# Kernel tuning notes

Hardware: AMD Instinct MI355X
Metric: run time of the kernel (lower is better)

## Reference

```python
import jax, jax.numpy as jnp
import numpy as np

NUM_USERS = 100000
NUM_ITEMS = 50000
N_NODES = NUM_USERS + NUM_ITEMS
EMBED_K = 64
N_LAYERS = 3
N_EDGES = 2000000
BATCH = 4096
EPS = 1e-12
NEG_SLOPE = 0.01  # torch.nn.functional.leaky_relu default


def setup_inputs() -> dict:
    key = jax.random.key(0)
    ks = jax.random.split(key, 12)
    return {
        "Gu": jax.random.normal(ks[0], (NUM_USERS, EMBED_K), jnp.float32) * 0.1,
        "Gi": jax.random.normal(ks[1], (NUM_ITEMS, EMBED_K), jnp.float32) * 0.1,
        "W1": jax.random.normal(ks[2], (N_LAYERS, EMBED_K, EMBED_K), jnp.float32) * 0.1,
        "b1": jax.random.normal(ks[3], (N_LAYERS, EMBED_K), jnp.float32) * 0.1,
        "W2": jax.random.normal(ks[4], (N_LAYERS, EMBED_K, EMBED_K), jnp.float32) * 0.1,
        "b2": jax.random.normal(ks[5], (N_LAYERS, EMBED_K), jnp.float32) * 0.1,
        "edge_w": jax.random.uniform(ks[6], (N_EDGES,), jnp.float32),
        "edge_src": jax.random.randint(ks[7], (N_EDGES,), 0, N_NODES, jnp.int32),
        "edge_dst": jax.random.randint(ks[8], (N_EDGES,), 0, N_NODES, jnp.int32),
        "user": jax.random.randint(ks[9], (BATCH,), 0, NUM_USERS, jnp.int32),
        "pos": jax.random.randint(ks[10], (BATCH,), 0, NUM_ITEMS, jnp.int32),
    }


def _propagate(Gu, Gi, W1, b1, W2, b2, edge_w, edge_src, edge_dst):
    # ego embeddings: concat users then items -> [N, d]
    x = jnp.concatenate([Gu, Gi], axis=0)
    embs = [x]
    for l in range(N_LAYERS):
        xj = x[edge_src]                       # [E, d] source (neighbor) feats
        xi = x[edge_dst]                       # [E, d] destination feats
        # NGCF message: norm * (lin1(x_j) + lin2(x_j * x_i))
        msg = (xj @ W1[l] + b1[l]) + ((xj * xi) @ W2[l] + b2[l])
        msg = msg * edge_w[:, None]
        agg = jax.ops.segment_sum(msg, edge_dst, num_segments=N_NODES)
        # update: aggregated messages + self transform, then LeakyReLU
        out = jax.nn.leaky_relu(agg + x @ W1[l] + b1[l], negative_slope=NEG_SLOPE)
        # message dropout is identity in eval mode; then row-wise L2 normalize
        nrm = jnp.sqrt(jnp.sum(out * out, axis=1, keepdims=True))
        x = out / jnp.maximum(nrm, EPS)
        embs.append(x)
    all_e = jnp.concatenate(embs, axis=1)      # [N, d*(L+1)]
    return all_e[:NUM_USERS], all_e[NUM_USERS:]


def reference(Gu, Gi, W1, b1, W2, b2, edge_w, edge_src, edge_dst, user, pos):
    gu, gi = _propagate(Gu, Gi, W1, b1, W2, b2, edge_w, edge_src, edge_dst)
    gamma_u = gu[user]                         # [B, d*(L+1)]
    gamma_i = gi[pos]
    xui = jnp.sum(gamma_u * gamma_i, axis=1)   # [B]
    return xui
```

## Files before the change

### kernel.cpp

```cpp
#include <hip/hip_runtime.h>


#define SCAN_TILE 4096

__global__ __launch_bounds__(256) void init_x_kernel(
    const float* __restrict__ Gu, const float* __restrict__ Gi,
    float* __restrict__ x, int nu4, int nt4) {
  int i = blockIdx.x * 256 + threadIdx.x;
  if (i >= nt4) return;
  float4 v = (i < nu4) ? ((const float4*)Gu)[i] : ((const float4*)Gi)[i - nu4];
  ((float4*)x)[i] = v;
}

__global__ __launch_bounds__(256) void hist_kernel(
    const int* __restrict__ dst, int* __restrict__ counts, int E) {
  int e = blockIdx.x * 256 + threadIdx.x;
  if (e >= E) return;
  atomicAdd(&counts[dst[e]], 1);
}

__global__ __launch_bounds__(256) void tile_sum_kernel(
    const int* __restrict__ counts, int* __restrict__ tsum, int n) {
  int tid = threadIdx.x;
  int lo = blockIdx.x * SCAN_TILE + tid * 16;
  int s = 0;
  if (lo + 16 <= n) {
    const int4* p = (const int4*)(counts + lo);
#pragma unroll
    for (int q = 0; q < 4; ++q) {
      int4 v = p[q];
      s += v.x + v.y + v.z + v.w;
    }
  } else {
    for (int i = lo; i < n && i < lo + 16; ++i) s += counts[i];
  }
#pragma unroll
  for (int m = 1; m < 64; m <<= 1) s += __shfl_xor(s, m, 64);
  __shared__ int red[4];
  if ((tid & 63) == 0) red[tid >> 6] = s;
  __syncthreads();
  if (tid == 0) tsum[blockIdx.x] = red[0] + red[1] + red[2] + red[3];
}

__global__ __launch_bounds__(64) void tile_scan_kernel(int* __restrict__ tsum,
                                                       int ntiles) {
  int lane = threadIdx.x;
  if (ntiles <= 64) {
    int v = (lane < ntiles) ? tsum[lane] : 0;
    int incl = v;
#pragma unroll
    for (int m = 1; m < 64; m <<= 1) {
      int t = __shfl_up(incl, m, 64);
      if (lane >= m) incl += t;
    }
    if (lane < ntiles) tsum[lane] = incl - v;
  } else if (lane == 0) {
    int run = 0;
    for (int i = 0; i < ntiles; ++i) {
      int t = tsum[i];
      tsum[i] = run;
      run += t;
    }
  }
}

__global__ __launch_bounds__(256) void tile_write_kernel(
    const int* __restrict__ counts, const int* __restrict__ tsum,
    int* __restrict__ starts, int* __restrict__ cursor, int n) {
  int tid = threadIdx.x;
  int lo = blockIdx.x * SCAN_TILE + tid * 16;
  int c[16];
  int s = 0;
#pragma unroll
  for (int q = 0; q < 16; ++q) {
    int i = lo + q;
    int v = (i < n) ? counts[i] : 0;
    c[q] = v;
    s += v;
  }
  __shared__ int bs[256];
  bs[tid] = s;
  __syncthreads();
  int incl = s;
  for (int off = 1; off < 256; off <<= 1) {
    int t = (tid >= off) ? bs[tid - off] : 0;
    __syncthreads();
    incl += t;
    bs[tid] = incl;
    __syncthreads();
  }
  int run = tsum[blockIdx.x] + incl - s;
#pragma unroll
  for (int q = 0; q < 16; ++q) {
    int i = lo + q;
    if (i < n) {
      starts[i] = run;
      cursor[i] = run;
      run += c[q];
    }
  }
}

__global__ __launch_bounds__(256) void place_kernel(
    const int* __restrict__ src, const int* __restrict__ dst,
    const float* __restrict__ w, int* __restrict__ cursor,
    int* __restrict__ ssrc, float* __restrict__ sw, int E) {
  int e = blockIdx.x * 256 + threadIdx.x;
  if (e >= E) return;
  int p = atomicAdd(&cursor[dst[e]], 1);
  ssrc[p] = src[e];
  sw[p] = w[e];
}

__global__ __launch_bounds__(256) void dot_kernel(
    const float* __restrict__ x, const int* __restrict__ user,
    const int* __restrict__ pos, float* __restrict__ out,
    int batch, int nusers, int accumulate) {
  int b = blockIdx.x * 4 + (threadIdx.x >> 6);
  int lane = threadIdx.x & 63;
  if (b >= batch) return;
  int u = user[b];
  int p = nusers + pos[b];
  float val = x[u * 64 + lane] * x[p * 64 + lane];
#pragma unroll
  for (int m = 1; m < 64; m <<= 1) val += __shfl_xor(val, m, 64);
  if (lane == 0) out[b] = accumulate ? (out[b] + val) : val;
}

__global__ __launch_bounds__(256) void layer_kernel(
    const float* __restrict__ xc, float* __restrict__ xn,
    const float* __restrict__ W1, const float* __restrict__ b1,
    const float* __restrict__ W2, const float* __restrict__ b2,
    const int* __restrict__ starts, const int* __restrict__ degs,
    const int* __restrict__ ssrc, const float* __restrict__ sw, int nnodes) {
  const int lane = threadIdx.x & 63;
  const int wid = threadIdx.x >> 6;
  __shared__ float ash[4][64];
  __shared__ float gsh[4][64];

  float w1c[64], w2c[64];
#pragma unroll
  for (int j = 0; j < 64; ++j) {
    w1c[j] = W1[j * 64 + lane];
    w2c[j] = W2[j * 64 + lane];
  }
  const float b1k = b1[lane];
  const float b2k = b2[lane];

  const int wstride = gridDim.x * 4;
  for (int v = blockIdx.x * 4 + wid; v < nnodes; v += wstride) {
    const float xk = xc[v * 64 + lane];
    int s0 = __builtin_amdgcn_readfirstlane(starts[v]);
    int dg = __builtin_amdgcn_readfirstlane(degs[v]);
    int nl = dg < 64 ? dg : 64;

    int myidx = 0;
    float myw = 0.f;
    if (lane < nl) {
      myidx = ssrc[s0 + lane] * 64;
      myw = sw[s0 + lane];
    }
    float wsum = myw;
#pragma unroll
    for (int m = 1; m < 64; m <<= 1) wsum += __shfl_xor(wsum, m, 64);

    float S = 0.f;
    int j = 0;
    for (; j + 8 <= nl; j += 8) {
      float vv[8], ww[8];
#pragma unroll
      for (int q = 0; q < 8; ++q) {
        int a = __builtin_amdgcn_readlane(myidx, j + q);
        ww[q] = __uint_as_float(
            __builtin_amdgcn_readlane(__float_as_uint(myw), j + q));
        vv[q] = xc[a + lane];
      }
#pragma unroll
      for (int q = 0; q < 8; ++q) S = fmaf(ww[q], vv[q], S);
    }
    for (; j < nl; ++j) {
      int a = __builtin_amdgcn_readlane(myidx, j);
      float w = __uint_as_float(
          __builtin_amdgcn_readlane(__float_as_uint(myw), j));
      S = fmaf(w, xc[a + lane], S);
    }
    for (int e = s0 + 64; e < s0 + dg; ++e) {
      float w = sw[e];
      wsum += w;
      S = fmaf(w, xc[ssrc[e] * 64 + lane], S);
    }

    ash[wid][lane] = S + xk;
    gsh[wid][lane] = S * xk;
    asm volatile("" ::: "memory");

    float acc1 = 0.f, acc2 = 0.f;
#pragma unroll
    for (int q = 0; q < 16; ++q) {
      float4 av, gv;
      __builtin_memcpy(&av, &ash[wid][4 * q], 16);
      __builtin_memcpy(&gv, &gsh[wid][4 * q], 16);
      acc1 = fmaf(av.x, w1c[4 * q + 0], acc1);
      acc1 = fmaf(av.y, w1c[4 * q + 1], acc1);
      acc1 = fmaf(av.z, w1c[4 * q + 2], acc1);
      acc1 = fmaf(av.w, w1c[4 * q + 3], acc1);
      acc2 = fmaf(gv.x, w2c[4 * q + 0], acc2);
      acc2 = fmaf(gv.y, w2c[4 * q + 1], acc2);
      acc2 = fmaf(gv.z, w2c[4 * q + 2], acc2);
      acc2 = fmaf(gv.w, w2c[4 * q + 3], acc2);
    }
    const float cv = wsum;
    float pre = acc1 + acc2 + (cv + 1.0f) * b1k + cv * b2k;
    float o = (pre > 0.0f) ? pre : 0.01f * pre;
    float ss = o * o;
#pragma unroll
    for (int m = 1; m < 64; m <<= 1) ss += __shfl_xor(ss, m, 64);
    float nrm = sqrtf(ss);
    xn[v * 64 + lane] = o / fmaxf(nrm, 1e-12f);
  }
}

extern "C" void kernel_launch(void* const* d_in, const int* in_sizes, int n_in,
                              void* d_out, int out_size, void* d_ws, size_t ws_size,
                              hipStream_t stream) {
  const float* Gu = (const float*)d_in[0];
  const float* Gi = (const float*)d_in[1];
  const float* W1 = (const float*)d_in[2];
  const float* b1 = (const float*)d_in[3];
  const float* W2 = (const float*)d_in[4];
  const float* b2 = (const float*)d_in[5];
  const float* ew = (const float*)d_in[6];
  const int* esrc = (const int*)d_in[7];
  const int* edst = (const int*)d_in[8];
  const int* user = (const int*)d_in[9];
  const int* pos = (const int*)d_in[10];
  float* out = (float*)d_out;

  const int NU = in_sizes[0] / 64;
  const int NI = in_sizes[1] / 64;
  const int N = NU + NI;
  const int E = in_sizes[6];
  const int B = in_sizes[9];

  char* ws = (char*)d_ws;
  size_t off = 0;
  auto carve = [&](size_t bytes) -> void* {
    void* p = ws + off;
    off = (off + bytes + 255) & ~(size_t)255;
    return p;
  };
  float* x0 = (float*)carve((size_t)N * 64 * 4);
  float* x1 = (float*)carve((size_t)N * 64 * 4);
  int* ssrc = (int*)carve((size_t)E * 4);
  float* sw = (float*)carve((size_t)E * 4);
  int* startsA = (int*)carve((size_t)N * 4);
  int* cursor = (int*)carve((size_t)N * 4);
  int* counts = (int*)carve((size_t)N * 4);
  const int ntiles = (N + SCAN_TILE - 1) / SCAN_TILE;
  int* tsum = (int*)carve((size_t)ntiles * 4);

  hipMemsetAsync(counts, 0, (size_t)N * 4, stream);

  hist_kernel<<<(E + 255) / 256, 256, 0, stream>>>(edst, counts, E);
  tile_sum_kernel<<<ntiles, 256, 0, stream>>>(counts, tsum, N);
  tile_scan_kernel<<<1, 64, 0, stream>>>(tsum, ntiles);
  tile_write_kernel<<<ntiles, 256, 0, stream>>>(counts, tsum, startsA, cursor, N);
  place_kernel<<<(E + 255) / 256, 256, 0, stream>>>(esrc, edst, ew, cursor, ssrc, sw, E);

  int nt4 = N * 64 / 4;
  int nu4 = NU * 64 / 4;
  init_x_kernel<<<(nt4 + 255) / 256, 256, 0, stream>>>(Gu, Gi, x0, nu4, nt4);
  dot_kernel<<<(B + 3) / 4, 256, 0, stream>>>(x0, user, pos, out, B, NU, 0);

  float* xc = x0;
  float* xn = x1;
  for (int l = 0; l < 3; ++l) {
    layer_kernel<<<768, 256, 0, stream>>>(xc, xn, W1 + l * 4096, b1 + l * 64,
                                          W2 + l * 4096, b2 + l * 64, startsA,
                                          counts, ssrc, sw, N);
    dot_kernel<<<(B + 3) / 4, 256, 0, stream>>>(xn, user, pos, out, B, NU, 1);
    float* t = xc;
    xc = xn;
    xn = t;
  }
}
```

Measured before the change: 927.7 us.

## Pack edge src/weight into int2 and gather with float4 per quarter-wave

Merges the separate sorted source-index and weight arrays into one interleaved int2 buffer, so each edge record is fetched in a single load. The per-node aggregation is restructured so that each 16-lane group of a wavefront handles one edge and loads a full 64-float row as float4s. A wave therefore processes four edges per gather step, and the partial sums are combined with cross-group shuffles. This is meant to raise memory-level parallelism and vector load width in the neighbor gather, at the cost of extra shuffle reductions and a shared-memory write limited to 16 lanes.

Measured after the change: 1.266 ms. +36.5%, slower.

```diff
diff --git a/kernel.cpp b/kernel.cpp
--- a/kernel.cpp
+++ b/kernel.cpp
@@ -104,12 +104,11 @@
 __global__ __launch_bounds__(256) void place_kernel(
     const int* __restrict__ src, const int* __restrict__ dst,
     const float* __restrict__ w, int* __restrict__ cursor,
-    int* __restrict__ ssrc, float* __restrict__ sw, int E) {
+    int2* __restrict__ ebuf, int E) {
   int e = blockIdx.x * 256 + threadIdx.x;
   if (e >= E) return;
   int p = atomicAdd(&cursor[dst[e]], 1);
-  ssrc[p] = src[e];
-  sw[p] = w[e];
+  ebuf[p] = make_int2(src[e], __float_as_int(w[e]));
 }
 
 __global__ __launch_bounds__(256) void dot_kernel(
@@ -132,9 +131,11 @@
     const float* __restrict__ W1, const float* __restrict__ b1,
     const float* __restrict__ W2, const float* __restrict__ b2,
     const int* __restrict__ starts, const int* __restrict__ degs,
-    const int* __restrict__ ssrc, const float* __restrict__ sw, int nnodes) {
+    const int2* __restrict__ ebuf, int nnodes) {
   const int lane = threadIdx.x & 63;
   const int wid = threadIdx.x >> 6;
+  const int es = lane >> 4;
+  const int ds = lane & 15;
   __shared__ float ash[4][64];
   __shared__ float gsh[4][64];
 
@@ -149,49 +150,52 @@
 
   const int wstride = gridDim.x * 4;
   for (int v = blockIdx.x * 4 + wid; v < nnodes; v += wstride) {
-    const float xk = xc[v * 64 + lane];
-    int s0 = __builtin_amdgcn_readfirstlane(starts[v]);
-    int dg = __builtin_amdgcn_readfirstlane(degs[v]);
-    int nl = dg < 64 ? dg : 64;
-
-    int myidx = 0;
-    float myw = 0.f;
-    if (lane < nl) {
-      myidx = ssrc[s0 + lane] * 64;
-      myw = sw[s0 + lane];
-    }
-    float wsum = myw;
-#pragma unroll
-    for (int m = 1; m < 64; m <<= 1) wsum += __shfl_xor(wsum, m, 64);
-
-    float S = 0.f;
-    int j = 0;
-    for (; j + 8 <= nl; j += 8) {
-      float vv[8], ww[8];
-#pragma unroll
-      for (int q = 0; q < 8; ++q) {
-        int a = __builtin_amdgcn_readlane(myidx, j + q);
-        ww[q] = __uint_as_float(
-            __builtin_amdgcn_readlane(__float_as_uint(myw), j + q));
-        vv[q] = xc[a + lane];
+    const int e0 = __builtin_amdgcn_readfirstlane(starts[v]);
+    const int dg = __builtin_amdgcn_readfirstlane(degs[v]);
+
+    float4 S4 = make_float4(0.f, 0.f, 0.f, 0.f);
+    float wacc = 0.f;
+    for (int base = 0; base < dg; base += 16) {
+      int idx[4];
+      float wv[4];
+#pragma unroll
+      for (int r = 0; r < 4; ++r) {
+        int e = base + r * 4 + es;
+        int2 m = (e < dg) ? ebuf[e0 + e] : make_int2(0, 0);
+        idx[r] = m.x << 6;
+        wv[r] = __int_as_float(m.y);
       }
-#pragma unroll
-      for (int q = 0; q < 8; ++q) S = fmaf(ww[q], vv[q], S);
-    }
-    for (; j < nl; ++j) {
-      int a = __builtin_amdgcn_readlane(myidx, j);
-      float w = __uint_as_float(
-          __builtin_amdgcn_readlane(__float_as_uint(myw), j));
-      S = fmaf(w, xc[a + lane], S);
-    }
-    for (int e = s0 + 64; e < s0 + dg; ++e) {
-      float w = sw[e];
-      wsum += w;
-      S = fmaf(w, xc[ssrc[e] * 64 + lane], S);
-    }
-
-    ash[wid][lane] = S + xk;
-    gsh[wid][lane] = S * xk;
+      float4 g[4];
+#pragma unroll
+      for (int r = 0; r < 4; ++r)
+        g[r] = *(const float4*)(xc + idx[r] + ds * 4);
+#pragma unroll
+      for (int r = 0; r < 4; ++r) {
+        S4.x = fmaf(wv[r], g[r].x, S4.x);
+        S4.y = fmaf(wv[r], g[r].y, S4.y);
+        S4.z = fmaf(wv[r], g[r].z, S4.z);
+        S4.w = fmaf(wv[r], g[r].w, S4.w);
+        wacc += wv[r];
+      }
+    }
+#pragma unroll
+    for (int m = 16; m < 64; m <<= 1) {
+      S4.x += __shfl_xor(S4.x, m, 64);
+      S4.y += __shfl_xor(S4.y, m, 64);
+      S4.z += __shfl_xor(S4.z, m, 64);
+      S4.w += __shfl_xor(S4.w, m, 64);
+      wacc += __shfl_xor(wacc, m, 64);
+    }
+
+    const float4 xk4 = *(const float4*)(xc + v * 64 + ds * 4);
+    if (lane < 16) {
+      float4 av = make_float4(S4.x + xk4.x, S4.y + xk4.y, S4.z + xk4.z,
+                              S4.w + xk4.w);
+      float4 gv = make_float4(S4.x * xk4.x, S4.y * xk4.y, S4.z * xk4.z,
+                              S4.w * xk4.w);
+      *(float4*)&ash[wid][lane * 4] = av;
+      *(float4*)&gsh[wid][lane * 4] = gv;
+    }
     asm volatile("" ::: "memory");
 
     float acc1 = 0.f, acc2 = 0.f;
@@ -209,7 +213,7 @@
       acc2 = fmaf(gv.z, w2c[4 * q + 2], acc2);
       acc2 = fmaf(gv.w, w2c[4 * q + 3], acc2);
     }
-    const float cv = wsum;
+    const float cv = wacc;
     float pre = acc1 + acc2 + (cv + 1.0f) * b1k + cv * b2k;
     float o = (pre > 0.0f) ? pre : 0.01f * pre;
     float ss = o * o;
@@ -251,8 +255,7 @@
   };
   float* x0 = (float*)carve((size_t)N * 64 * 4);
   float* x1 = (float*)carve((size_t)N * 64 * 4);
-  int* ssrc = (int*)carve((size_t)E * 4);
-  float* sw = (float*)carve((size_t)E * 4);
+  int2* ebuf = (int2*)carve((size_t)E * 8);
   int* startsA = (int*)carve((size_t)N * 4);
   int* cursor = (int*)carve((size_t)N * 4);
   int* counts = (int*)carve((size_t)N * 4);
@@ -265,7 +268,7 @@
   tile_sum_kernel<<<ntiles, 256, 0, stream>>>(counts, tsum, N);
   tile_scan_kernel<<<1, 64, 0, stream>>>(tsum, ntiles);
   tile_write_kernel<<<ntiles, 256, 0, stream>>>(counts, tsum, startsA, cursor, N);
-  place_kernel<<<(E + 255) / 256, 256, 0, stream>>>(esrc, edst, ew, cursor, ssrc, sw, E);
+  place_kernel<<<(E + 255) / 256, 256, 0, stream>>>(esrc, edst, ew, cursor, ebuf, E);
 
   int nt4 = N * 64 / 4;
   int nu4 = NU * 64 / 4;
@@ -277,7 +280,7 @@
   for (int l = 0; l < 3; ++l) {
     layer_kernel<<<768, 256, 0, stream>>>(xc, xn, W1 + l * 4096, b1 + l * 64,
                                           W2 + l * 4096, b2 + l * 64, startsA,
-                                          counts, ssrc, sw, N);
+                                          counts, ebuf, N);
     dot_kernel<<<(B + 3) / 4, 256, 0, stream>>>(xn, user, pos, out, B, NU, 1);
     float* t = xc;
     xc = xn;
```

## Interleave edge source and weight into int2 buffer and double layer grid

Applied to the files above, without the earlier changes.

Packs each sorted edge's source index and weight into a single int2 array, so the scatter writes and the layer kernel's edge reads each use one 8-byte access instead of two separate arrays. The layer kernel's launch grid grows from 768 to 1536 blocks, and the grid-stride uses a compile-time constant. The packing is meant to cut memory transactions and scattered writes in the place step. The larger grid adds more waves for latency hiding but repeats the per-block load of W1/W2 into registers more often.

New measurement: 931.6 us. No clear change (+0.4%).

```diff
diff --git a/kernel.cpp b/kernel.cpp
--- a/kernel.cpp
+++ b/kernel.cpp
@@ -2,6 +2,7 @@
 
 
 #define SCAN_TILE 4096
+#define LAYER_GRID 1536
 
 __global__ __launch_bounds__(256) void init_x_kernel(
     const float* __restrict__ Gu, const float* __restrict__ Gi,
@@ -104,12 +105,11 @@
 __global__ __launch_bounds__(256) void place_kernel(
     const int* __restrict__ src, const int* __restrict__ dst,
     const float* __restrict__ w, int* __restrict__ cursor,
-    int* __restrict__ ssrc, float* __restrict__ sw, int E) {
+    int2* __restrict__ ebuf, int E) {
   int e = blockIdx.x * 256 + threadIdx.x;
   if (e >= E) return;
   int p = atomicAdd(&cursor[dst[e]], 1);
-  ssrc[p] = src[e];
-  sw[p] = w[e];
+  ebuf[p] = make_int2(src[e], __float_as_int(w[e]));
 }
 
 __global__ __launch_bounds__(256) void dot_kernel(
@@ -132,7 +132,7 @@
     const float* __restrict__ W1, const float* __restrict__ b1,
     const float* __restrict__ W2, const float* __restrict__ b2,
     const int* __restrict__ starts, const int* __restrict__ degs,
-    const int* __restrict__ ssrc, const float* __restrict__ sw, int nnodes) {
+    const int2* __restrict__ ebuf, int nnodes) {
   const int lane = threadIdx.x & 63;
   const int wid = threadIdx.x >> 6;
   __shared__ float ash[4][64];
@@ -147,7 +147,7 @@
   const float b1k = b1[lane];
   const float b2k = b2[lane];
 
-  const int wstride = gridDim.x * 4;
+  const int wstride = LAYER_GRID * 4;
   for (int v = blockIdx.x * 4 + wid; v < nnodes; v += wstride) {
     const float xk = xc[v * 64 + lane];
     int s0 = __builtin_amdgcn_readfirstlane(starts[v]);
@@ -157,8 +157,9 @@
     int myidx = 0;
     float myw = 0.f;
     if (lane < nl) {
-      myidx = ssrc[s0 + lane] * 64;
-      myw = sw[s0 + lane];
+      int2 m = ebuf[s0 + lane];
+      myidx = m.x << 6;
+      myw = __int_as_float(m.y);
     }
     float wsum = myw;
 #pragma unroll
@@ -185,9 +186,10 @@
       S = fmaf(w, xc[a + lane], S);
     }
     for (int e = s0 + 64; e < s0 + dg; ++e) {
-      float w = sw[e];
+      int2 m = ebuf[e];
+      float w = __int_as_float(m.y);
       wsum += w;
-      S = fmaf(w, xc[ssrc[e] * 64 + lane], S);
+      S = fmaf(w, xc[(m.x << 6) + lane], S);
     }
 
     ash[wid][lane] = S + xk;
@@ -251,8 +253,7 @@
   };
   float* x0 = (float*)carve((size_t)N * 64 * 4);
   float* x1 = (float*)carve((size_t)N * 64 * 4);
-  int* ssrc = (int*)carve((size_t)E * 4);
-  float* sw = (float*)carve((size_t)E * 4);
+  int2* ebuf = (int2*)carve((size_t)E * 8);
   int* startsA = (int*)carve((size_t)N * 4);
   int* cursor = (int*)carve((size_t)N * 4);
   int* counts = (int*)carve((size_t)N * 4);
@@ -265,7 +266,7 @@
   tile_sum_kernel<<<ntiles, 256, 0, stream>>>(counts, tsum, N);
   tile_scan_kernel<<<1, 64, 0, stream>>>(tsum, ntiles);
   tile_write_kernel<<<ntiles, 256, 0, stream>>>(counts, tsum, startsA, cursor, N);
-  place_kernel<<<(E + 255) / 256, 256, 0, stream>>>(esrc, edst, ew, cursor, ssrc, sw, E);
+  place_kernel<<<(E + 255) / 256, 256, 0, stream>>>(esrc, edst, ew, cursor, ebuf, E);
 
   int nt4 = N * 64 / 4;
   int nu4 = NU * 64 / 4;
@@ -275,9 +276,10 @@
   float* xc = x0;
   float* xn = x1;
   for (int l = 0; l < 3; ++l) {
-    layer_kernel<<<768, 256, 0, stream>>>(xc, xn, W1 + l * 4096, b1 + l * 64,
-                                          W2 + l * 4096, b2 + l * 64, startsA,
-                                          counts, ssrc, sw, N);
+    layer_kernel<<<LAYER_GRID, 256, 0, stream>>>(xc, xn, W1 + l * 4096,
+                                                 b1 + l * 64, W2 + l * 4096,
+                                                 b2 + l * 64, startsA, counts,
+                                                 ebuf, N);
     dot_kernel<<<(B + 3) / 4, 256, 0, stream>>>(xn, user, pos, out, B, NU, 1);
     float* t = xc;
     xc = xn;
```
